# Performance work log

Measured on AMD Instinct MI355X. Metric: run time of the kernel, lower is better.

Reference implementation:

```python
import jax, jax.numpy as jnp
import numpy as np

WINDOW_SIZE = 64  # matches init_kwargs


def _local_allowed_mask(L, window_size):
    # Original torch code: for query i, keys in slice [max(i-w//2,0) : min(i+w//2, L)) are allowed.
    half = window_size // 2
    i = jnp.arange(L)[:, None]
    j = jnp.arange(L)[None, :]
    return (j >= i - half) & (j < i + half)  # [L, L] bool, True = attend


def setup_inputs() -> dict:
    key = jax.random.key(0)
    kq, kk, kv = jax.random.split(key, 3)
    B, L, H, E, D = 4, 2048, 16, 64, 64
    queries = jax.random.normal(kq, (B, L, H, E), dtype=jnp.float32)
    keys = jax.random.normal(kk, (B, L, H, E), dtype=jnp.float32)
    values = jax.random.normal(kv, (B, L, H, D), dtype=jnp.float32)
    attn_mask = jnp.zeros((1,), dtype=bool)  # unused by the module
    return {"queries": queries, "keys": keys, "values": values, "attn_mask": attn_mask}


def reference(queries, keys, values, attn_mask):
    B, L, H, E = queries.shape
    scale = 1.0 / np.sqrt(E).astype(np.float32)
    allowed = _local_allowed_mask(L, WINDOW_SIZE)  # [L, L]
    # Dense scores, as in the original module (einsum 'blhe,bshe->bhls')
    scores = jnp.einsum('blhe,bshe->bhls', queries, keys)
    neg_inf = jnp.asarray(-jnp.inf, dtype=scores.dtype)
    scores = jnp.where(allowed[None, None, :, :], scores, neg_inf)
    A = jax.nn.softmax(scale * scores, axis=-1)  # [B, H, L, S]
    V = jnp.einsum('bhls,bshd->blhd', A, values)  # [B, L, H, D]
    return V
```

## Files before the change

kernel.cpp:

```cpp
#include <hip/hip_runtime.h>


#define B_ 4
#define L_ 2048
#define H_ 16
#define E_ 64
#define D_ 64
#define KS_STRIDE 72
#define VT_STRIDE 152
#define P_STRIDE 104

typedef __attribute__((ext_vector_type(8))) short short8;
typedef __attribute__((ext_vector_type(4))) float f32x4;

__device__ __forceinline__ unsigned int f2bf(float x) {
  unsigned int b = __float_as_uint(x);
  b += 0x7fffu + ((b >> 16) & 1u);
  return b >> 16;
}
__device__ __forceinline__ unsigned int pack2(float a, float b) {
  return f2bf(a) | (f2bf(b) << 16);
}
__device__ __forceinline__ short8 pack8(const float4& a, const float4& b) {
  union { short8 s; uint4 u; } r;
  r.u = make_uint4(pack2(a.x, a.y), pack2(a.z, a.w), pack2(b.x, b.y), pack2(b.z, b.w));
  return r.s;
}

__global__ __launch_bounds__(256, 3)
void local_attn_mfma(const float* __restrict__ qg,
                     const float* __restrict__ kg,
                     const float* __restrict__ vg,
                     float* __restrict__ og) {
  __shared__ __align__(16) unsigned short Ks[128 * KS_STRIDE];
  __shared__ __align__(16) unsigned short Vt[64 * VT_STRIDE];
  __shared__ __align__(16) unsigned short Pl[4 * 16 * P_STRIDE];

  const int t = threadIdx.x;
  const int q0 = blockIdx.x * 64;
  const int h = blockIdx.y;
  const int b = blockIdx.z;
  const int kstart = q0 - 32;
  const int wave = t >> 6;
  const int lane = t & 63;
  const int col16 = lane & 15;
  const int quad = lane >> 4;

  const float4 fzero = make_float4(0.f, 0.f, 0.f, 0.f);

  float4 kf[8];
  #pragma unroll
  for (int it = 0; it < 8; ++it) {
    int cid = t + it * 256;
    int row = cid >> 4, ch = cid & 15;
    int key = kstart + row;
    kf[it] = (key >= 0 && key < L_)
      ? *(const float4*)(kg + ((size_t)(b * L_ + key) * H_ + h) * E_ + ch * 4)
      : fzero;
  }
  const int kp = t >> 2;
  const int dq = t & 3;
  float4 va[4], vc[4];
  {
    int k0 = kstart + 2 * kp, k1 = k0 + 1;
    #pragma unroll
    for (int i = 0; i < 4; ++i) { va[i] = fzero; vc[i] = fzero; }
    if (k0 >= 0 && k0 < L_) {
      const float* p = vg + ((size_t)(b * L_ + k0) * H_ + h) * D_ + dq * 16;
      #pragma unroll
      for (int i = 0; i < 4; ++i) va[i] = *(const float4*)(p + i * 4);
    }
    if (k1 >= 0 && k1 < L_) {
      const float* p = vg + ((size_t)(b * L_ + k1) * H_ + h) * D_ + dq * 16;
      #pragma unroll
      for (int i = 0; i < 4; ++i) vc[i] = *(const float4*)(p + i * 4);
    }
  }
  float4 qf0, qf1, qf2, qf3;
  {
    const float* p = qg + ((size_t)(b * L_ + q0 + wave * 16 + col16) * H_ + h) * E_ + quad * 8;
    qf0 = *(const float4*)p;
    qf1 = *(const float4*)(p + 4);
    qf2 = *(const float4*)(p + 32);
    qf3 = *(const float4*)(p + 36);
  }

  #pragma unroll
  for (int it = 0; it < 8; ++it) {
    int cid = t + it * 256;
    int row = cid >> 4, ch = cid & 15;
    float4 f = kf[it];
    *(uint2*)&Ks[row * KS_STRIDE + ch * 4] = make_uint2(pack2(f.x, f.y), pack2(f.z, f.w));
  }
  #pragma unroll
  for (int i = 0; i < 4; ++i) {
    float av[4] = {va[i].x, va[i].y, va[i].z, va[i].w};
    float cv[4] = {vc[i].x, vc[i].y, vc[i].z, vc[i].w};
    #pragma unroll
    for (int j = 0; j < 4; ++j) {
      int d = dq * 16 + i * 4 + j;
      *(unsigned int*)&Vt[d * VT_STRIDE + 2 * kp] = pack2(av[j], cv[j]);
    }
  }
  *(uint2*)&Vt[(t >> 2) * VT_STRIDE + 128 + (t & 3) * 4] = make_uint2(0u, 0u);

  const short8 qa0 = pack8(qf0, qf1);
  const short8 qa1 = pack8(qf2, qf3);
  __syncthreads();

  f32x4 acc[5];
  #pragma unroll
  for (int tt = 0; tt < 5; ++tt) {
    int krow = wave * 16 + tt * 16 + col16;
    short8 b0 = *(const short8*)&Ks[krow * KS_STRIDE + quad * 8];
    short8 b1 = *(const short8*)&Ks[krow * KS_STRIDE + quad * 8 + 32];
    f32x4 c = {0.f, 0.f, 0.f, 0.f};
    c = __builtin_amdgcn_mfma_f32_16x16x32_bf16(qa0, b0, c, 0, 0, 0);
    c = __builtin_amdgcn_mfma_f32_16x16x32_bf16(qa1, b1, c, 0, 0, 0);
    acc[tt] = c;
  }

  #pragma unroll
  for (int r = 0; r < 4; ++r) {
    const int row_loc = quad * 4 + r;
    float x[5];
    #pragma unroll
    for (int tt = 0; tt < 5; ++tt) {
      int c_loc = tt * 16 + col16;
      int gkey = kstart + wave * 16 + c_loc;
      bool ok = (c_loc >= row_loc) && (c_loc < row_loc + 64) && (gkey >= 0) && (gkey < L_);
      x[tt] = ok ? acc[tt][r] * 0.125f : -1e30f;
    }
    float m = fmaxf(fmaxf(fmaxf(x[0], x[1]), fmaxf(x[2], x[3])), x[4]);
    m = fmaxf(m, __shfl_xor(m, 1));
    m = fmaxf(m, __shfl_xor(m, 2));
    m = fmaxf(m, __shfl_xor(m, 4));
    m = fmaxf(m, __shfl_xor(m, 8));
    float s = 0.f;
    #pragma unroll
    for (int tt = 0; tt < 5; ++tt) { x[tt] = __expf(x[tt] - m); s += x[tt]; }
    s += __shfl_xor(s, 1);
    s += __shfl_xor(s, 2);
    s += __shfl_xor(s, 4);
    s += __shfl_xor(s, 8);
    float inv = 1.0f / s;
    #pragma unroll
    for (int tt = 0; tt < 5; ++tt) acc[tt][r] = x[tt] * inv;
  }

  unsigned short* Pw = &Pl[wave * 16 * P_STRIDE];
  *(uint2*)&Pw[col16 * P_STRIDE + 80 + quad * 4] = make_uint2(0u, 0u);
  #pragma unroll
  for (int tt = 0; tt < 5; ++tt)
    #pragma unroll
    for (int r = 0; r < 4; ++r)
      Pw[(quad * 4 + r) * P_STRIDE + tt * 16 + col16] = (unsigned short)f2bf(acc[tt][r]);

  f32x4 oacc[4];
  #pragma unroll
  for (int nt = 0; nt < 4; ++nt) oacc[nt] = (f32x4){0.f, 0.f, 0.f, 0.f};
  #pragma unroll
  for (int ks = 0; ks < 3; ++ks) {
    short8 pa = *(const short8*)&Pw[col16 * P_STRIDE + ks * 32 + quad * 8];
    #pragma unroll
    for (int nt = 0; nt < 4; ++nt) {
      short8 vb = *(const short8*)&Vt[(nt * 16 + col16) * VT_STRIDE + wave * 16 + ks * 32 + quad * 8];
      oacc[nt] = __builtin_amdgcn_mfma_f32_16x16x32_bf16(pa, vb, oacc[nt], 0, 0, 0);
    }
  }

  #pragma unroll
  for (int r = 0; r < 4; ++r) {
    int q = q0 + wave * 16 + quad * 4 + r;
    float* orow = og + ((size_t)(b * L_ + q) * H_ + h) * D_;
    #pragma unroll
    for (int nt = 0; nt < 4; ++nt)
      orow[nt * 16 + col16] = oacc[nt][r];
  }
}

extern "C" void kernel_launch(void* const* d_in, const int* in_sizes, int n_in,
                              void* d_out, int out_size, void* d_ws, size_t ws_size,
                              hipStream_t stream) {
  const float* q = (const float*)d_in[0];
  const float* k = (const float*)d_in[1];
  const float* v = (const float*)d_in[2];
  float* o = (float*)d_out;
  dim3 grid(L_ / 64, H_, B_);
  local_attn_mfma<<<grid, dim3(256), 0, stream>>>(q, k, v, o);
}
```

Measured before the change: 141.4 us.

## Process four query tiles per block with register prefetch of next tile

```diff
diff --git a/kernel.cpp b/kernel.cpp
--- a/kernel.cpp
+++ b/kernel.cpp
@@ -9,6 +9,7 @@
 #define KS_STRIDE 72
 #define VT_STRIDE 152
 #define P_STRIDE 104
+#define NTILES 4
 
 typedef __attribute__((ext_vector_type(8))) short short8;
 typedef __attribute__((ext_vector_type(4))) float f32x4;
@@ -26,8 +27,11 @@
   r.u = make_uint4(pack2(a.x, a.y), pack2(a.z, a.w), pack2(b.x, b.y), pack2(b.z, b.w));
   return r.s;
 }
-
-__global__ __launch_bounds__(256, 3)
+__device__ __forceinline__ void barrier_lgkm() {
+  asm volatile("s_waitcnt lgkmcnt(0)\n\ts_barrier" ::: "memory");
+}
+
+__global__ __launch_bounds__(256, 2)
 void local_attn_mfma(const float* __restrict__ qg,
                      const float* __restrict__ kg,
                      const float* __restrict__ vg,
@@ -37,32 +41,31 @@
   __shared__ __align__(16) unsigned short Pl[4 * 16 * P_STRIDE];
 
   const int t = threadIdx.x;
-  const int q0 = blockIdx.x * 64;
+  const int qbase = blockIdx.x * (NTILES * 64);
   const int h = blockIdx.y;
   const int b = blockIdx.z;
-  const int kstart = q0 - 32;
   const int wave = t >> 6;
   const int lane = t & 63;
   const int col16 = lane & 15;
   const int quad = lane >> 4;
-
-  const float4 fzero = make_float4(0.f, 0.f, 0.f, 0.f);
-
-  float4 kf[8];
-  #pragma unroll
-  for (int it = 0; it < 8; ++it) {
-    int cid = t + it * 256;
-    int row = cid >> 4, ch = cid & 15;
-    int key = kstart + row;
-    kf[it] = (key >= 0 && key < L_)
-      ? *(const float4*)(kg + ((size_t)(b * L_ + key) * H_ + h) * E_ + ch * 4)
-      : fzero;
-  }
   const int kp = t >> 2;
   const int dq = t & 3;
-  float4 va[4], vc[4];
-  {
-    int k0 = kstart + 2 * kp, k1 = k0 + 1;
+  const float4 fzero = make_float4(0.f, 0.f, 0.f, 0.f);
+
+  float4 kf[8], va[4], vc[4], qf[4];
+
+  auto load_tile = [&](int q0) {
+    const int ks0 = q0 - 32;
+    #pragma unroll
+    for (int itr = 0; itr < 8; ++itr) {
+      int cid = t + itr * 256;
+      int row = cid >> 4, ch = cid & 15;
+      int key = ks0 + row;
+      kf[itr] = (key >= 0 && key < L_)
+        ? *(const float4*)(kg + ((size_t)(b * L_ + key) * H_ + h) * E_ + ch * 4)
+        : fzero;
+    }
+    int k0 = ks0 + 2 * kp, k1 = k0 + 1;
     #pragma unroll
     for (int i = 0; i < 4; ++i) { va[i] = fzero; vc[i] = fzero; }
     if (k0 >= 0 && k0 < L_) {
@@ -75,107 +78,117 @@
       #pragma unroll
       for (int i = 0; i < 4; ++i) vc[i] = *(const float4*)(p + i * 4);
     }
-  }
-  float4 qf0, qf1, qf2, qf3;
-  {
     const float* p = qg + ((size_t)(b * L_ + q0 + wave * 16 + col16) * H_ + h) * E_ + quad * 8;
-    qf0 = *(const float4*)p;
-    qf1 = *(const float4*)(p + 4);
-    qf2 = *(const float4*)(p + 32);
-    qf3 = *(const float4*)(p + 36);
-  }
+    qf[0] = *(const float4*)p;
+    qf[1] = *(const float4*)(p + 4);
+    qf[2] = *(const float4*)(p + 32);
+    qf[3] = *(const float4*)(p + 36);
+  };
+
+  load_tile(qbase);
 
   #pragma unroll
-  for (int it = 0; it < 8; ++it) {
-    int cid = t + it * 256;
-    int row = cid >> 4, ch = cid & 15;
-    float4 f = kf[it];
-    *(uint2*)&Ks[row * KS_STRIDE + ch * 4] = make_uint2(pack2(f.x, f.y), pack2(f.z, f.w));
-  }
-  #pragma unroll
-  for (int i = 0; i < 4; ++i) {
-    float av[4] = {va[i].x, va[i].y, va[i].z, va[i].w};
-    float cv[4] = {vc[i].x, vc[i].y, vc[i].z, vc[i].w};
-    #pragma unroll
-    for (int j = 0; j < 4; ++j) {
-      int d = dq * 16 + i * 4 + j;
-      *(unsigned int*)&Vt[d * VT_STRIDE + 2 * kp] = pack2(av[j], cv[j]);
-    }
-  }
-  *(uint2*)&Vt[(t >> 2) * VT_STRIDE + 128 + (t & 3) * 4] = make_uint2(0u, 0u);
-
-  const short8 qa0 = pack8(qf0, qf1);
-  const short8 qa1 = pack8(qf2, qf3);
-  __syncthreads();
-
-  f32x4 acc[5];
-  #pragma unroll
-  for (int tt = 0; tt < 5; ++tt) {
-    int krow = wave * 16 + tt * 16 + col16;
-    short8 b0 = *(const short8*)&Ks[krow * KS_STRIDE + quad * 8];
-    short8 b1 = *(const short8*)&Ks[krow * KS_STRIDE + quad * 8 + 32];
-    f32x4 c = {0.f, 0.f, 0.f, 0.f};
-    c = __builtin_amdgcn_mfma_f32_16x16x32_bf16(qa0, b0, c, 0, 0, 0);
-    c = __builtin_amdgcn_mfma_f32_16x16x32_bf16(qa1, b1, c, 0, 0, 0);
-    acc[tt] = c;
-  }
-
-  #pragma unroll
-  for (int r = 0; r < 4; ++r) {
-    const int row_loc = quad * 4 + r;
-    float x[5];
+  for (int it = 0; it < NTILES; ++it) {
+    const int q0 = qbase + it * 64;
+    const int kstart = q0 - 32;
+
+    #pragma unroll
+    for (int itr = 0; itr < 8; ++itr) {
+      int cid = t + itr * 256;
+      int row = cid >> 4, ch = cid & 15;
+      float4 f = kf[itr];
+      *(uint2*)&Ks[row * KS_STRIDE + ch * 4] = make_uint2(pack2(f.x, f.y), pack2(f.z, f.w));
+    }
+    #pragma unroll
+    for (int i = 0; i < 4; ++i) {
+      float av[4] = {va[i].x, va[i].y, va[i].z, va[i].w};
+      float cv[4] = {vc[i].x, vc[i].y, vc[i].z, vc[i].w};
+      #pragma unroll
+      for (int j = 0; j < 4; ++j) {
+        int d = dq * 16 + i * 4 + j;
+        *(unsigned int*)&Vt[d * VT_STRIDE + 2 * kp] = pack2(av[j], cv[j]);
+      }
+    }
+    *(uint2*)&Vt[(t >> 2) * VT_STRIDE + 128 + (t & 3) * 4] = make_uint2(0u, 0u);
+
+    const short8 qa0 = pack8(qf[0], qf[1]);
+    const short8 qa1 = pack8(qf[2], qf[3]);
+
+    barrier_lgkm();
+
+    if (it + 1 < NTILES) load_tile(qbase + (it + 1) * 64);
+
+    f32x4 acc[5];
     #pragma unroll
     for (int tt = 0; tt < 5; ++tt) {
-      int c_loc = tt * 16 + col16;
-      int gkey = kstart + wave * 16 + c_loc;
-      bool ok = (c_loc >= row_loc) && (c_loc < row_loc + 64) && (gkey >= 0) && (gkey < L_);
-      x[tt] = ok ? acc[tt][r] * 0.125f : -1e30f;
-    }
-    float m = fmaxf(fmaxf(fmaxf(x[0], x[1]), fmaxf(x[2], x[3])), x[4]);
-    m = fmaxf(m, __shfl_xor(m, 1));
-    m = fmaxf(m, __shfl_xor(m, 2));
-    m = fmaxf(m, __shfl_xor(m, 4));
-    m = fmaxf(m, __shfl_xor(m, 8));
-    float s = 0.f;
-    #pragma unroll
-    for (int tt = 0; tt < 5; ++tt) { x[tt] = __expf(x[tt] - m); s += x[tt]; }
-    s += __shfl_xor(s, 1);
-    s += __shfl_xor(s, 2);
-    s += __shfl_xor(s, 4);
-    s += __shfl_xor(s, 8);
-    float inv = 1.0f / s;
-    #pragma unroll
-    for (int tt = 0; tt < 5; ++tt) acc[tt][r] = x[tt] * inv;
-  }
-
-  unsigned short* Pw = &Pl[wave * 16 * P_STRIDE];
-  *(uint2*)&Pw[col16 * P_STRIDE + 80 + quad * 4] = make_uint2(0u, 0u);
-  #pragma unroll
-  for (int tt = 0; tt < 5; ++tt)
-    #pragma unroll
-    for (int r = 0; r < 4; ++r)
-      Pw[(quad * 4 + r) * P_STRIDE + tt * 16 + col16] = (unsigned short)f2bf(acc[tt][r]);
-
-  f32x4 oacc[4];
-  #pragma unroll
-  for (int nt = 0; nt < 4; ++nt) oacc[nt] = (f32x4){0.f, 0.f, 0.f, 0.f};
-  #pragma unroll
-  for (int ks = 0; ks < 3; ++ks) {
-    short8 pa = *(const short8*)&Pw[col16 * P_STRIDE + ks * 32 + quad * 8];
-    #pragma unroll
-    for (int nt = 0; nt < 4; ++nt) {
-      short8 vb = *(const short8*)&Vt[(nt * 16 + col16) * VT_STRIDE + wave * 16 + ks * 32 + quad * 8];
-      oacc[nt] = __builtin_amdgcn_mfma_f32_16x16x32_bf16(pa, vb, oacc[nt], 0, 0, 0);
-    }
-  }
-
-  #pragma unroll
-  for (int r = 0; r < 4; ++r) {
-    int q = q0 + wave * 16 + quad * 4 + r;
-    float* orow = og + ((size_t)(b * L_ + q) * H_ + h) * D_;
-    #pragma unroll
-    for (int nt = 0; nt < 4; ++nt)
-      orow[nt * 16 + col16] = oacc[nt][r];
+      int krow = wave * 16 + tt * 16 + col16;
+      short8 b0 = *(const short8*)&Ks[krow * KS_STRIDE + quad * 8];
+      short8 b1 = *(const short8*)&Ks[krow * KS_STRIDE + quad * 8 + 32];
+      f32x4 c = {0.f, 0.f, 0.f, 0.f};
+      c = __builtin_amdgcn_mfma_f32_16x16x32_bf16(qa0, b0, c, 0, 0, 0);
+      c = __builtin_amdgcn_mfma_f32_16x16x32_bf16(qa1, b1, c, 0, 0, 0);
+      acc[tt] = c;
+    }
+
+    #pragma unroll
+    for (int r = 0; r < 4; ++r) {
+      const int row_loc = quad * 4 + r;
+      float x[5];
+      #pragma unroll
+      for (int tt = 0; tt < 5; ++tt) {
+        int c_loc = tt * 16 + col16;
+        int gkey = kstart + wave * 16 + c_loc;
+        bool ok = (c_loc >= row_loc) && (c_loc < row_loc + 64) && (gkey >= 0) && (gkey < L_);
+        x[tt] = ok ? acc[tt][r] * 0.125f : -1e30f;
+      }
+      float m = fmaxf(fmaxf(fmaxf(x[0], x[1]), fmaxf(x[2], x[3])), x[4]);
+      m = fmaxf(m, __shfl_xor(m, 1));
+      m = fmaxf(m, __shfl_xor(m, 2));
+      m = fmaxf(m, __shfl_xor(m, 4));
+      m = fmaxf(m, __shfl_xor(m, 8));
+      float s = 0.f;
+      #pragma unroll
+      for (int tt = 0; tt < 5; ++tt) { x[tt] = __expf(x[tt] - m); s += x[tt]; }
+      s += __shfl_xor(s, 1);
+      s += __shfl_xor(s, 2);
+      s += __shfl_xor(s, 4);
+      s += __shfl_xor(s, 8);
+      float inv = 1.0f / s;
+      #pragma unroll
+      for (int tt = 0; tt < 5; ++tt) acc[tt][r] = x[tt] * inv;
+    }
+
+    unsigned short* Pw = &Pl[wave * 16 * P_STRIDE];
+    *(uint2*)&Pw[col16 * P_STRIDE + 80 + quad * 4] = make_uint2(0u, 0u);
+    #pragma unroll
+    for (int tt = 0; tt < 5; ++tt)
+      #pragma unroll
+      for (int r = 0; r < 4; ++r)
+        Pw[(quad * 4 + r) * P_STRIDE + tt * 16 + col16] = (unsigned short)f2bf(acc[tt][r]);
+
+    f32x4 oacc[4];
+    #pragma unroll
+    for (int nt = 0; nt < 4; ++nt) oacc[nt] = (f32x4){0.f, 0.f, 0.f, 0.f};
+    #pragma unroll
+    for (int ks = 0; ks < 3; ++ks) {
+      short8 pa = *(const short8*)&Pw[col16 * P_STRIDE + ks * 32 + quad * 8];
+      #pragma unroll
+      for (int nt = 0; nt < 4; ++nt) {
+        short8 vb = *(const short8*)&Vt[(nt * 16 + col16) * VT_STRIDE + wave * 16 + ks * 32 + quad * 8];
+        oacc[nt] = __builtin_amdgcn_mfma_f32_16x16x32_bf16(pa, vb, oacc[nt], 0, 0, 0);
+      }
+    }
+
+    #pragma unroll
+    for (int r = 0; r < 4; ++r) {
+      int q = q0 + wave * 16 + quad * 4 + r;
+      float* orow = og + ((size_t)(b * L_ + q) * H_ + h) * D_;
+      #pragma unroll
+      for (int nt = 0; nt < 4; ++nt)
+        orow[nt * 16 + col16] = oacc[nt][r];
+    }
+
+    barrier_lgkm();
   }
 }
 
@@ -186,6 +199,6 @@
   const float* k = (const float*)d_in[1];
   const float* v = (const float*)d_in[2];
   float* o = (float*)d_out;
-  dim3 grid(L_ / 64, H_, B_);
+  dim3 grid(L_ / (NTILES * 64), H_, B_);
   local_attn_mfma<<<grid, dim3(256), 0, stream>>>(q, k, v, o);
 }
```

New measurement: 147.8 us. 1.05x slower.
